# Performance work log

Measured on AMD Instinct MI355X. Metric: run time of the kernel, lower is better.

Reference implementation:

```python
import jax, jax.numpy as jnp
import numpy as np
from jax import lax

SD = 16  # sample_duration
POOL_KS = (SD, SD * 3 // 4, SD // 2, SD // 4)  # (16, 12, 8, 4)


def conv3d_same(x, w, b):
    # x: [B,C,T,H,W], w: [O,I,3,3,3]
    y = lax.conv_general_dilated(
        x, w, window_strides=(1, 1, 1), padding=[(1, 1), (1, 1), (1, 1)],
        dimension_numbers=("NCDHW", "OIDHW", "NCDHW"))
    return y + b[None, :, None, None, None]


def maxpool_t(x, k):
    # MaxPool3d((k,1,1), stride=1): max over sliding temporal window
    return lax.reduce_window(x, -jnp.inf, lax.max,
                             (1, 1, k, 1, 1), (1, 1, 1, 1, 1), "VALID")


def head1x1(x, w, b):
    # 1x1x1 Conv3d as einsum; x: [B,C,T,H,W], w: [O,C]
    return jnp.einsum("bcthw,oc->bothw", x, w) + b[None, :, None, None, None]


def cls_prob(score):
    # _RPN.reshape(x,2) -> softmax(dim=1) -> reshape back to [B,30,T,H,W]
    B, C, T, H, W = score.shape
    s2 = score.reshape(B, 2, (C * T) // 2, H, W)
    p = jax.nn.softmax(s2, axis=1)
    return p.reshape(B, C, T, H, W)


def setup_inputs() -> dict:
    key = jax.random.key(0)
    ks = jax.random.split(key, 12)
    din, B, H, W = 512, 2, 28, 28
    s = 0.05
    return {
        "base_feat": jax.random.normal(ks[0], (B, din, SD, H, W), jnp.float32),
        "im_info": jnp.ones((B, 3), jnp.float32) * 448.0,
        "gt_boxes": jax.random.uniform(ks[1], (B, 20, 5), jnp.float32),
        "gt_rois": jax.random.uniform(ks[2], (B, 20, SD, 5), jnp.float32),
        "W_conv": jax.random.normal(ks[3], (din, din, 3, 3, 3), jnp.float32) * 0.01,
        "b_conv": jnp.zeros((din,), jnp.float32),
        "W_cls": jax.random.normal(ks[4], (30, din), jnp.float32) * s,
        "b_cls": jnp.zeros((30,), jnp.float32),
        "W_bbox": jax.random.normal(ks[5], (960, din), jnp.float32) * s,
        "b_bbox": jnp.zeros((960,), jnp.float32),
        "W_bbox_34": jax.random.normal(ks[6], (720, din), jnp.float32) * s,
        "b_bbox_34": jnp.zeros((720,), jnp.float32),
        "W_bbox_2": jax.random.normal(ks[7], (480, din), jnp.float32) * s,
        "b_bbox_2": jnp.zeros((480,), jnp.float32),
        "W_bbox_4": jax.random.normal(ks[8], (240, din), jnp.float32) * s,
        "b_bbox_4": jnp.zeros((240,), jnp.float32),
    }


def reference(base_feat, im_info, gt_boxes, gt_rois,
              W_conv, b_conv, W_cls, b_cls,
              W_bbox, b_bbox, W_bbox_34, b_bbox_34,
              W_bbox_2, b_bbox_2, W_bbox_4, b_bbox_4):
    # RPN conv + relu
    x = jax.nn.relu(conv3d_same(base_feat, W_conv, b_conv))
    # four temporal max-pool branches (T' = 1, 5, 9, 13)
    pools = [maxpool_t(x, k) for k in POOL_KS]
    # NOTE: original code applies the SAME RPN_cls_score conv to all branches
    probs = tuple(cls_prob(head1x1(p, W_cls, b_cls)) for p in pools)
    bbox_ws = [(W_bbox, b_bbox), (W_bbox_34, b_bbox_34),
               (W_bbox_2, b_bbox_2), (W_bbox_4, b_bbox_4)]
    bboxes = tuple(head1x1(p, w, b) for p, (w, b) in zip(pools, bbox_ws))
    return probs + bboxes
```

## Files before the change

kernel.cpp:

```cpp
#include <hip/hip_runtime.h>

typedef unsigned short u16;
typedef unsigned int   u32;
typedef __bf16  bf16x8 __attribute__((ext_vector_type(8)));
typedef float   f32x4  __attribute__((ext_vector_type(4)));

__device__ __forceinline__ float bf2f(u16 u) {
    u32 v = ((u32)u) << 16;
    return __builtin_bit_cast(float, v);
}
__device__ __forceinline__ u16 f2bf(float f) {
    u32 u = __builtin_bit_cast(u32, f);
    return (u16)((u + 0x7FFFu + ((u >> 16) & 1u)) >> 16);
}
__device__ __forceinline__ float ldf(const void* p, long i, int f32) {
    return f32 ? ((const float*)p)[i] : bf2f(((const u16*)p)[i]);
}
__device__ __forceinline__ int is_f32(const u32* im) {
    return im[0] == 0x43E00000u;
}
__device__ __forceinline__ void gl2lds16(const u16* g, u16* l) {
    __builtin_amdgcn_global_load_lds(
        (const __attribute__((address_space(1))) void*)g,
        (__attribute__((address_space(3))) void*)l, 16, 0, 0);
}

__global__ void zero_halo(u16* __restrict__ xpad)
{
    int i = blockIdx.x * 256 + threadIdx.x;
    if (i < 230400) {
        int c8 = i & 63; int pos = i >> 6;
        int p = pos % 900; pos /= 900;
        int t = (pos & 1) * 17; int b = pos >> 1;
        long o = (((long)(b * 18 + t) * 900) + p) * 512 + c8 * 8;
        *(uint4*)&xpad[o] = uint4{0u, 0u, 0u, 0u};
        return;
    }
    i -= 230400;
    if (i < 122880) {
        int c8 = i & 63; int pos = i >> 6;
        int w = pos % 30; pos /= 30;
        int h = (pos & 1) * 29; pos >>= 1;
        int t = pos % 16 + 1; int b = pos / 16;
        long o = ((((long)(b * 18 + t) * 30 + h) * 30) + w) * 512 + c8 * 8;
        *(uint4*)&xpad[o] = uint4{0u, 0u, 0u, 0u};
        return;
    }
    i -= 122880;
    if (i < 114688) {
        int c8 = i & 63; int pos = i >> 6;
        int w = (pos & 1) * 29; pos >>= 1;
        int h = pos % 28 + 1; pos /= 28;
        int t = pos % 16 + 1; int b = pos / 16;
        long o = ((((long)(b * 18 + t) * 30 + h) * 30) + w) * 512 + c8 * 8;
        *(uint4*)&xpad[o] = uint4{0u, 0u, 0u, 0u};
    }
}

__global__ void pad_fill(const void* __restrict__ src, u16* __restrict__ xpad,
                         const u32* __restrict__ im)
{
    const int f32 = is_f32(im);
    __shared__ u16 lds[56 * 40];
    int blk = blockIdx.x;
    const int h2  = blk % 14;  blk /= 14;
    const int c32 = blk & 15;  blk >>= 4;
    const int t   = blk & 15;
    const int b   = blk >> 4;
    const int tid = threadIdx.x;
    const long sbase = ((long)(b * 512 + c32 * 32) * 16 + t) * 784 + h2 * 56;
    #pragma unroll
    for (int it = tid; it < 1792; it += 256) {
        const int c = it / 56, p = it - c * 56;
        float v = f32 ? ((const float*)src)[sbase + (long)c * 12544 + p]
                      : bf2f(((const u16*)src)[sbase + (long)c * 12544 + p]);
        lds[p * 40 + c] = f2bf(v);
    }
    __syncthreads();
    if (tid < 224) {
        const int p = tid >> 2, g = tid & 3;
        const int h = h2 * 2 + p / 28, w = p % 28;
        const long o = (((long)(b * 18 + t + 1) * 30 + h + 1) * 30 + (w + 1)) * 512
                       + c32 * 32 + g * 8;
        *(uint4*)&xpad[o] = *(const uint4*)&lds[p * 40 + g * 8];
    }
}

__global__ void wt_transform(const void* __restrict__ wconv, u16* __restrict__ wt,
                             const u32* __restrict__ im)
{
    const int f32 = is_f32(im);
    __shared__ u16 lds[256 * 28];
    const int tid = threadIdx.x;
    const int pair_base = blockIdx.x * 256;
    const long s0 = (long)pair_base * 27;
    for (int it = tid; it < 256 * 27; it += 256) {
        const int p = it / 27, o = it - p * 27;
        float v = f32 ? ((const float*)wconv)[s0 + it]
                      : bf2f(((const u16*)wconv)[s0 + it]);
        lds[p * 28 + o] = f2bf(v);
    }
    __syncthreads();
    #pragma unroll
    for (int off = 0; off < 27; ++off)
        wt[(long)off * 262144 + pair_base + tid] = lds[tid * 28 + off];
}

__global__ void cvt_all(const void* s0, const void* s1, const void* s2,
                        const void* s3, const void* s4,
                        const void* b0, const void* b1, const void* b2,
                        const void* b3, const void* b4, const void* b5,
                        u16* __restrict__ whd, float* __restrict__ bfs,
                        const u32* __restrict__ im)
{
    const int f32 = is_f32(im);
    int i = blockIdx.x * 256 + threadIdx.x;
    if (i < 1244160) {
        const void* s; long j;
        if      (i < 15360)   { s = s0; j = i; }
        else if (i < 506880)  { s = s1; j = i - 15360; }
        else if (i < 875520)  { s = s2; j = i - 506880; }
        else if (i < 1121280) { s = s3; j = i - 875520; }
        else                  { s = s4; j = i - 1121280; }
        whd[i] = f2bf(ldf(s, j, f32));
        return;
    }
    i -= 1244160;
    if (i >= 2942) return;
    float v;
    if      (i < 512)  v = ldf(b0, i, f32);
    else if (i < 542)  v = ldf(b1, i - 512, f32);
    else if (i < 1502) v = ldf(b2, i - 542, f32);
    else if (i < 2222) v = ldf(b3, i - 1502, f32);
    else if (i < 2702) v = ldf(b4, i - 2222, f32);
    else               v = ldf(b5, i - 2702, f32);
    bfs[i] = v;
}

__global__ __launch_bounds__(512, 2) void conv_gemm256(
    const u16* __restrict__ xpad, const u16* __restrict__ wt,
    const float* __restrict__ bfs, u16* __restrict__ y)
{
    __shared__ u16 smem[65536];
    const int tid = threadIdx.x;

    const int bx  = blockIdx.x;
    const int xcd = bx & 7, pos = bx >> 3;
    const int L   = (xcd < 4 ? xcd * 25 : 100 + (xcd - 4) * 24) + pos;
    const int m_base = (L & 1) * 256;
    const int n_base = (L >> 1) * 256;

    const int rq8 = tid >> 3;
    const int sw  = (((tid & 7) ^ (rq8 & 7))) * 8;
    const u16* pa = wt + (long)(m_base + rq8) * 512 + sw;

    long sbj[4];
    #pragma unroll
    for (int j = 0; j < 4; ++j) {
        const int n = n_base + j * 64 + rq8;
        int b = n / 12544, r = n % 12544;
        int t = r / 784,   q = r % 784;
        int h = q / 28,    w = q % 28;
        const int sa = ((b * 18 + t) * 30 + h) * 30 + w;
        sbj[j] = (long)sa * 512 + sw;
    }

    const int lane = tid & 63, wid = tid >> 6;
    const int l16 = lane & 15, quad = lane >> 4;
    const int wm = wid >> 2;
    const int wn = wid & 3;
    const int x7 = l16 & 7;
    const int o0 = (quad ^ x7) * 8;
    const int o1 = ((4 + quad) ^ x7) * 8;
    int rowA[8], rowB[4];
    #pragma unroll
    for (int mi = 0; mi < 8; ++mi) rowA[mi] = (wm * 128 + mi * 16 + l16) * 64;
    #pragma unroll
    for (int ni = 0; ni < 4; ++ni) rowB[ni] = 16384 + (wn * 64 + ni * 16 + l16) * 64;

    f32x4 acc[8][4] = {};

    {
        u16* dst = smem;
        #pragma unroll
        for (int j = 0; j < 4; ++j)
            gl2lds16(pa + (long)j * 32768, dst + j * 4096 + tid * 8);
        #pragma unroll
        for (int j = 0; j < 4; ++j)
            gl2lds16(xpad + sbj[j], dst + 16384 + j * 4096 + tid * 8);
    }

    for (int kt = 0; kt < 216; ++kt) {
        asm volatile("s_waitcnt vmcnt(0)" ::: "memory");
        asm volatile("s_barrier" ::: "memory");
        const u16* buf = smem + (kt & 1) * 32768;

        bf16x8 af[8], bfr[4];
        #pragma unroll
        for (int mi = 0; mi < 4; ++mi)
            af[mi] = *(const bf16x8*)&buf[rowA[mi] + o0];
        #pragma unroll
        for (int ni = 0; ni < 4; ++ni)
            bfr[ni] = *(const bf16x8*)&buf[rowB[ni] + o0];
        #pragma unroll
        for (int mi = 4; mi < 8; ++mi)
            af[mi] = *(const bf16x8*)&buf[rowA[mi] + o0];

        if (kt < 215) {
            const int kts = kt + 1;
            const int tap = kts >> 3, kc = kts & 7;
            const int kd = tap / 9, r9 = tap - kd * 9;
            const int kh = r9 / 3,  kw = r9 - kh * 3;
            const long aoff = (long)tap * 262144 + kc * 64;
            const long boff = (long)(kd * 900 + kh * 30 + kw) * 512 + kc * 64;
            u16* dst = smem + ((kts & 1) << 15);
            #pragma unroll
            for (int j = 0; j < 4; ++j)
                gl2lds16(pa + aoff + (long)j * 32768, dst + j * 4096 + tid * 8);
            #pragma unroll
            for (int j = 0; j < 4; ++j)
                gl2lds16(xpad + sbj[j] + boff, dst + 16384 + j * 4096 + tid * 8);
        }

        __builtin_amdgcn_s_setprio(1);
        #pragma unroll
        for (int mi = 0; mi < 8; ++mi)
            #pragma unroll
            for (int ni = 0; ni < 4; ++ni)
                acc[mi][ni] = __builtin_amdgcn_mfma_f32_16x16x32_bf16(
                    af[mi], bfr[ni], acc[mi][ni], 0, 0, 0);
        __builtin_amdgcn_s_setprio(0);

        bf16x8 ag[8], bgr[4];
        #pragma unroll
        for (int mi = 0; mi < 8; ++mi)
            ag[mi] = *(const bf16x8*)&buf[rowA[mi] + o1];
        #pragma unroll
        for (int ni = 0; ni < 4; ++ni)
            bgr[ni] = *(const bf16x8*)&buf[rowB[ni] + o1];

        __builtin_amdgcn_s_setprio(1);
        #pragma unroll
        for (int mi = 0; mi < 8; ++mi)
            #pragma unroll
            for (int ni = 0; ni < 4; ++ni)
                acc[mi][ni] = __builtin_amdgcn_mfma_f32_16x16x32_bf16(
                    ag[mi], bgr[ni], acc[mi][ni], 0, 0, 0);
        __builtin_amdgcn_s_setprio(0);
    }

    #pragma unroll
    for (int mi = 0; mi < 8; ++mi) {
        const int mrow = m_base + wm * 128 + mi * 16 + quad * 4;
        float bias[4];
        #pragma unroll
        for (int r = 0; r < 4; ++r) bias[r] = bfs[mrow + r];
        #pragma unroll
        for (int ni = 0; ni < 4; ++ni) {
            const int ng = n_base + wn * 64 + ni * 16 + l16;
            f32x4 a = acc[mi][ni];
            u16 o0v = f2bf(fmaxf(a[0] + bias[0], 0.f));
            u16 o1v = f2bf(fmaxf(a[1] + bias[1], 0.f));
            u16 o2v = f2bf(fmaxf(a[2] + bias[2], 0.f));
            u16 o3v = f2bf(fmaxf(a[3] + bias[3], 0.f));
            uint2 pv;
            pv.x = (u32)o0v | ((u32)o1v << 16);
            pv.y = (u32)o2v | ((u32)o3v << 16);
            *(uint2*)&y[(long)ng * 512 + mrow] = pv;
        }
    }
}

__device__ __forceinline__ uint2 max4(uint2 A, uint2 Bv)
{
    const u16* a = (const u16*)&A;
    const u16* b = (const u16*)&Bv;
    uint2 R;
    u16* r = (u16*)&R;
    #pragma unroll
    for (int i = 0; i < 4; ++i) r[i] = (bf2f(a[i]) >= bf2f(b[i])) ? a[i] : b[i];
    return R;
}

__global__ void pool_all(const u16* __restrict__ y, u16* __restrict__ p4,
                         u16* __restrict__ p8, u16* __restrict__ p12,
                         u16* __restrict__ p16)
{
    int g = blockIdx.x * 256 + threadIdx.x;
    if (g >= 200704) return;
    const int c4 = g & 127;
    int pos = g >> 7;
    const int hw = pos % 784; const int b = pos / 784;
    const u16* src = y + ((long)(b * 16) * 784 + hw) * 512 + c4 * 4;
    uint2 v[16];
    #pragma unroll
    for (int t = 0; t < 16; ++t)
        v[t] = *(const uint2*)(src + (long)t * 401408);
    uint2 pr[15];
    #pragma unroll
    for (int t = 0; t < 15; ++t) pr[t] = max4(v[t], v[t + 1]);
    uint2 qd[13];
    #pragma unroll
    for (int t = 0; t < 13; ++t) qd[t] = max4(pr[t], pr[t + 2]);
    uint2 e8[9];
    #pragma unroll
    for (int t = 0; t < 9; ++t) e8[t] = max4(qd[t], qd[t + 4]);
    uint2 e12[5];
    #pragma unroll
    for (int t = 0; t < 5; ++t) e12[t] = max4(e8[t], qd[t + 8]);
    uint2 e16 = max4(e8[0], e8[8]);

    const long col = (long)hw * 512 + c4 * 4;
    #pragma unroll
    for (int t = 0; t < 13; ++t)
        *(uint2*)&p4[((long)(b * 13 + t) * 784) * 512 + col] = qd[t];
    #pragma unroll
    for (int t = 0; t < 9; ++t)
        *(uint2*)&p8[((long)(b * 9 + t) * 784) * 512 + col] = e8[t];
    #pragma unroll
    for (int t = 0; t < 5; ++t)
        *(uint2*)&p12[((long)(b * 5 + t) * 784) * 512 + col] = e12[t];
    *(uint2*)&p16[((long)b * 784) * 512 + col] = e16;
}

__global__ __launch_bounds__(256, 2) void heads_gemm(
    const u16* __restrict__ p16, const u16* __restrict__ p12,
    const u16* __restrict__ p8,  const u16* __restrict__ p4,
    const u16* __restrict__ wcls, const u16* __restrict__ wb1,
    const u16* __restrict__ wb34, const u16* __restrict__ wb2,
    const u16* __restrict__ wb4,  const float* __restrict__ bfs,
    float* __restrict__ clsr, void* __restrict__ outv,
    const u32* __restrict__ im)
{
    const int f32 = is_f32(im);
    int bid = blockIdx.x;
    const u16* pool; const u16* wbp; int Ti, CH, nt, mt; long boff, coff, ooff;
    if (bid < 104)      {             nt = bid % 13;  mt = bid / 13;  pool = p16; wbp = wb1;  Ti = 1;  CH = 960; boff = 542;  coff = 0;      ooff = 1317120; }
    else if (bid < 476) { bid -= 104; nt = bid % 62;  mt = bid / 62;  pool = p12; wbp = wb34; Ti = 5;  CH = 720; boff = 1502; coff = 47040;  ooff = 2822400; }
    else if (bid < 920) { bid -= 476; nt = bid % 111; mt = bid / 111; pool = p8;  wbp = wb2;  Ti = 9;  CH = 480; boff = 2222; coff = 282240; ooff = 8467200; }
    else                { bid -= 920; nt = bid % 160; mt = bid / 160; pool = p4;  wbp = wb4;  Ti = 13; CH = 240; boff = 2702; coff = 705600; ooff = 15240960; }
    const int M = 30 + CH;
    const int THW = Ti * 784;
    const int N = 2 * THW;
    const int n_base = nt * 128;
    const int m_base = mt * 128;

    __shared__ u16 lds_a[128 * 64];
    __shared__ u16 lds_b[128 * 64];
    const int tid = threadIdx.x;
    const int lane = tid & 63;
    const int wid  = tid >> 6;
    const int quad = lane >> 4;
    const int l16  = lane & 15;
    const int wm = (wid & 1) * 64;
    const int wn = (wid >> 1) * 64;
    const int srow = tid >> 3;
    const int lc8  = ((tid & 7) ^ (srow & 7)) * 8;

    const u16* arow[4]; const u16* brow[4];
    #pragma unroll
    for (int j = 0; j < 4; ++j) {
        int m = m_base + j * 32 + srow; if (m > M - 1) m = M - 1;
        arow[j] = ((m < 30) ? (wcls + m * 512) : (wbp + (m - 30) * 512)) + lc8;
        int n = n_base + j * 32 + srow; if (n > N - 1) n = N - 1;
        brow[j] = pool + (long)n * 512 + lc8;
    }

    u16* ldst_a = &lds_a[tid * 8];
    u16* ldst_b = &lds_b[tid * 8];

    int rowA[4], rowB[4];
    #pragma unroll
    for (int i = 0; i < 4; ++i) {
        rowA[i] = (wm + i * 16 + l16) * 64;
        rowB[i] = (wn + i * 16 + l16) * 64;
    }
    const int cx  = l16 & 7;
    const int ch0 = (quad ^ cx) * 8;
    const int ch1 = ((4 + quad) ^ cx) * 8;

    f32x4 acc[4][4] = {};
    for (int kc = 0; kc < 8; ++kc) {
        const int kcol = kc * 64;
        #pragma unroll
        for (int j = 0; j < 4; ++j)
            gl2lds16(arow[j] + kcol, ldst_a + j * 2048);
        #pragma unroll
        for (int j = 0; j < 4; ++j)
            gl2lds16(brow[j] + kcol, ldst_b + j * 2048);
        __syncthreads();
        #pragma unroll
        for (int h = 0; h < 2; ++h) {
            const int co = h ? ch1 : ch0;
            bf16x8 af[4], bfr[4];
            #pragma unroll
            for (int mi = 0; mi < 4; ++mi)
                af[mi]  = *(const bf16x8*)&lds_a[rowA[mi] + co];
            #pragma unroll
            for (int ni = 0; ni < 4; ++ni)
                bfr[ni] = *(const bf16x8*)&lds_b[rowB[ni] + co];
            #pragma unroll
            for (int mi = 0; mi < 4; ++mi)
                #pragma unroll
                for (int ni = 0; ni < 4; ++ni)
                    acc[mi][ni] = __builtin_amdgcn_mfma_f32_16x16x32_bf16(
                        af[mi], bfr[ni], acc[mi][ni], 0, 0, 0);
        }
        __syncthreads();
    }
    const float* bcls = bfs + 512;
    const float* bb   = bfs + boff;
    #pragma unroll
    for (int mi = 0; mi < 4; ++mi) {
        const int mrow = m_base + wm + mi * 16 + quad * 4;
        #pragma unroll
        for (int ni = 0; ni < 4; ++ni) {
            const int ng = n_base + wn + ni * 16 + l16;
            if (ng >= N) continue;
            const int b  = ng / THW;
            const int rr = ng % THW;
            f32x4 a = acc[mi][ni];
            #pragma unroll
            for (int r = 0; r < 4; ++r) {
                const int m = mrow + r;
                if (m >= M) break;
                const float bias = (m < 30) ? bcls[m] : bb[m - 30];
                const float v = a[r] + bias;
                if (m < 30) {
                    clsr[coff + ((long)(b * 30 + m)) * THW + rr] = v;
                } else {
                    const long oi = ooff + ((long)(b * CH + (m - 30))) * THW + rr;
                    if (f32) ((float*)outv)[oi] = v;
                    else     ((u16*)outv)[oi]   = f2bf(v);
                }
            }
        }
    }
}

__global__ void softmax_all(const float* __restrict__ clsr,
                            void* __restrict__ outv, const u32* __restrict__ im)
{
    const int f32 = is_f32(im);
    int g = blockIdx.x * 256 + threadIdx.x;
    if (g >= 658560) return;
    int Ti; long off;
    if      (g < 23520)  { Ti = 1;  off = 0; }
    else if (g < 141120) { Ti = 5;  off = 47040;  g -= 23520; }
    else if (g < 352800) { Ti = 9;  off = 282240; g -= 141120; }
    else                 { Ti = 13; off = 705600; g -= 352800; }
    const int THW = Ti * 784;
    const int rr = g % THW;
    int r2 = g / THW;
    const int j = r2 % 15; const int b = r2 / 15;
    const long i0 = off + ((long)(b * 30 + j)) * THW + rr;
    const long i1 = off + ((long)(b * 30 + j + 15)) * THW + rr;
    const float s0 = clsr[i0], s1 = clsr[i1];
    const float mx = fmaxf(s0, s1);
    const float e0 = __expf(s0 - mx), e1 = __expf(s1 - mx);
    const float inv = 1.0f / (e0 + e1);
    if (f32) {
        ((float*)outv)[i0] = e0 * inv;
        ((float*)outv)[i1] = e1 * inv;
    } else {
        ((u16*)outv)[i0] = f2bf(e0 * inv);
        ((u16*)outv)[i1] = f2bf(e1 * inv);
    }
}

extern "C" void kernel_launch(void* const* d_in, const int* in_sizes, int n_in,
                              void* d_out, int out_size, void* d_ws, size_t ws_size,
                              hipStream_t stream)
{
    const void* base_feat = d_in[0];
    const u32*  im_info   = (const u32*)d_in[1];
    const void* W_conv    = d_in[4];
    const void* b_conv    = d_in[5];
    const void* W_cls     = d_in[6];
    const void* b_cls     = d_in[7];
    const void* W_bbox    = d_in[8];
    const void* b_bbox    = d_in[9];
    const void* W_bbox34  = d_in[10];
    const void* b_bbox34  = d_in[11];
    const void* W_bbox2   = d_in[12];
    const void* b_bbox2   = d_in[13];
    const void* W_bbox4   = d_in[14];
    const void* b_bbox4   = d_in[15];

    char* ws = (char*)d_ws;
    u16*   xpad = (u16*)  (ws + 0);
    u16*   wt   = (u16*)  (ws + 33177600);
    u16*   y    = (u16*)  (ws + 47333376);
    u16*   p4   = (u16*)  (ws + 73023488);
    u16*   p8   = (u16*)  (ws + 93896704);
    u16*   p12  = (u16*)  (ws + 108347392);
    u16*   p16  = (u16*)  (ws + 116375552);
    float* clsr = (float*)(ws + 117981184);
    u16*   whd  = (u16*)  (ws + 123249728);
    float* bfs  = (float*)(ws + 125738048);

    u16* w_cls_b  = whd;
    u16* w_b1_b   = whd + 15360;
    u16* w_b34_b  = whd + 506880;
    u16* w_b2_b   = whd + 875520;
    u16* w_b4_b   = whd + 1121280;

    zero_halo<<<1828, 256, 0, stream>>>(xpad);
    pad_fill<<<7168, 256, 0, stream>>>(base_feat, xpad, im_info);
    wt_transform<<<1024, 256, 0, stream>>>(W_conv, wt, im_info);
    cvt_all<<<4873, 256, 0, stream>>>(W_cls, W_bbox, W_bbox34, W_bbox2, W_bbox4,
                                      b_conv, b_cls, b_bbox, b_bbox34, b_bbox2,
                                      b_bbox4, whd, bfs, im_info);

    conv_gemm256<<<196, 512, 0, stream>>>(xpad, wt, bfs, y);

    pool_all<<<784, 256, 0, stream>>>(y, p4, p8, p12, p16);

    heads_gemm<<<1400, 256, 0, stream>>>(p16, p12, p8, p4,
                                         w_cls_b, w_b1_b, w_b34_b, w_b2_b, w_b4_b,
                                         bfs, clsr, d_out, im_info);

    softmax_all<<<2573, 256, 0, stream>>>(clsr, d_out, im_info);
}
```

Measured before the change: 573.1 us.

## Double-buffer LDS in head GEMM kernel with K-step 32 and prefetch

Replaces the single-buffered 64-wide K tiles of the 1x1 head GEMM with two 32-wide LDS buffers. The load for the next K step is issued while MFMAs run on the current one, and one barrier per iteration replaces the two syncthreads. It also changes the XOR swizzle to match the narrower tile and raises wave priority around the MFMA block. The aim is to hide global-to-LDS latency. The cost is twice as many loop iterations and barriers, and it relies on the global_load_lds writes being complete before the s_waitcnt vmcnt(0).

```diff
diff --git a/kernel.cpp b/kernel.cpp
--- a/kernel.cpp
+++ b/kernel.cpp
@@ -345,8 +345,7 @@
     const int n_base = nt * 128;
     const int m_base = mt * 128;
 
-    __shared__ u16 lds_a[128 * 64];
-    __shared__ u16 lds_b[128 * 64];
+    __shared__ u16 lds[16384];
     const int tid = threadIdx.x;
     const int lane = tid & 63;
     const int wid  = tid >> 6;
@@ -354,60 +353,66 @@
     const int l16  = lane & 15;
     const int wm = (wid & 1) * 64;
     const int wn = (wid >> 1) * 64;
-    const int srow = tid >> 3;
-    const int lc8  = ((tid & 7) ^ (srow & 7)) * 8;
-
-    const u16* arow[4]; const u16* brow[4];
-    #pragma unroll
-    for (int j = 0; j < 4; ++j) {
-        int m = m_base + j * 32 + srow; if (m > M - 1) m = M - 1;
-        arow[j] = ((m < 30) ? (wcls + m * 512) : (wbp + (m - 30) * 512)) + lc8;
-        int n = n_base + j * 32 + srow; if (n > N - 1) n = N - 1;
-        brow[j] = pool + (long)n * 512 + lc8;
-    }
-
-    u16* ldst_a = &lds_a[tid * 8];
-    u16* ldst_b = &lds_b[tid * 8];
-
+
+    const int srow = tid >> 2;
+    const int kk   = (((tid & 3) ^ ((tid >> 3) & 3))) * 8;
+
+    const u16* arow[2]; const u16* brow[2];
+    #pragma unroll
+    for (int i = 0; i < 2; ++i) {
+        int m = m_base + i * 64 + srow; if (m > M - 1) m = M - 1;
+        arow[i] = ((m < 30) ? (wcls + m * 512) : (wbp + (m - 30) * 512)) + kk;
+        int n = n_base + i * 64 + srow; if (n > N - 1) n = N - 1;
+        brow[i] = pool + (long)n * 512 + kk;
+    }
+
+    const int co = (quad ^ ((l16 >> 1) & 3)) * 8;
     int rowA[4], rowB[4];
     #pragma unroll
     for (int i = 0; i < 4; ++i) {
-        rowA[i] = (wm + i * 16 + l16) * 64;
-        rowB[i] = (wn + i * 16 + l16) * 64;
-    }
-    const int cx  = l16 & 7;
-    const int ch0 = (quad ^ cx) * 8;
-    const int ch1 = ((4 + quad) ^ cx) * 8;
+        rowA[i] = (wm + i * 16 + l16) * 32 + co;
+        rowB[i] = 4096 + (wn + i * 16 + l16) * 32 + co;
+    }
+
+    #pragma unroll
+    for (int i = 0; i < 2; ++i)
+        gl2lds16(arow[i], &lds[i * 2048 + tid * 8]);
+    #pragma unroll
+    for (int i = 0; i < 2; ++i)
+        gl2lds16(brow[i], &lds[4096 + i * 2048 + tid * 8]);
 
     f32x4 acc[4][4] = {};
-    for (int kc = 0; kc < 8; ++kc) {
-        const int kcol = kc * 64;
-        #pragma unroll
-        for (int j = 0; j < 4; ++j)
-            gl2lds16(arow[j] + kcol, ldst_a + j * 2048);
-        #pragma unroll
-        for (int j = 0; j < 4; ++j)
-            gl2lds16(brow[j] + kcol, ldst_b + j * 2048);
-        __syncthreads();
-        #pragma unroll
-        for (int h = 0; h < 2; ++h) {
-            const int co = h ? ch1 : ch0;
-            bf16x8 af[4], bfr[4];
-            #pragma unroll
-            for (int mi = 0; mi < 4; ++mi)
-                af[mi]  = *(const bf16x8*)&lds_a[rowA[mi] + co];
+    for (int kc = 0; kc < 16; ++kc) {
+        asm volatile("s_waitcnt vmcnt(0)" ::: "memory");
+        asm volatile("s_barrier" ::: "memory");
+        const u16* buf = lds + (kc & 1) * 8192;
+        bf16x8 af[4], bfr[4];
+        #pragma unroll
+        for (int mi = 0; mi < 4; ++mi)
+            af[mi]  = *(const bf16x8*)&buf[rowA[mi]];
+        #pragma unroll
+        for (int ni = 0; ni < 4; ++ni)
+            bfr[ni] = *(const bf16x8*)&buf[rowB[ni]];
+        if (kc < 15) {
+            const int kcol = (kc + 1) * 32;
+            u16* dst = lds + ((kc + 1) & 1) * 8192 + tid * 8;
+            #pragma unroll
+            for (int i = 0; i < 2; ++i)
+                gl2lds16(arow[i] + kcol, dst + i * 2048);
+            #pragma unroll
+            for (int i = 0; i < 2; ++i)
+                gl2lds16(brow[i] + kcol, dst + 4096 + i * 2048);
+        }
+        __builtin_amdgcn_s_setprio(1);
+        #pragma unroll
+        for (int mi = 0; mi < 4; ++mi)
             #pragma unroll
             for (int ni = 0; ni < 4; ++ni)
-                bfr[ni] = *(const bf16x8*)&lds_b[rowB[ni] + co];
-            #pragma unroll
-            for (int mi = 0; mi < 4; ++mi)
-                #pragma unroll
-                for (int ni = 0; ni < 4; ++ni)
-                    acc[mi][ni] = __builtin_amdgcn_mfma_f32_16x16x32_bf16(
-                        af[mi], bfr[ni], acc[mi][ni], 0, 0, 0);
-        }
-        __syncthreads();
-    }
+                acc[mi][ni] = __builtin_amdgcn_mfma_f32_16x16x32_bf16(
+                    af[mi], bfr[ni], acc[mi][ni], 0, 0, 0);
+        __builtin_amdgcn_s_setprio(0);
+    }
+
     const float* bcls = bfs + 512;
     const float* bb   = bfs + boff;
     #pragma unroll
```

After: 569.4 us. Within noise of the previous version (-0.6%).
